# Performance work log

Measured on AMD Instinct MI355X. Metric: run time of the kernel, lower is better.

The kernel has to match this reference:

```python
import jax, jax.numpy as jnp
import numpy as np

NUM_NODES = 50000
NUM_GRAPHS = 64
HIDDEN = 256
F_IN = 256
NUM_EDGES = 800000


def setup_inputs() -> dict:
    key = jax.random.key(0)
    ks = jax.random.split(key, 8)
    x = jax.random.normal(ks[0], (NUM_NODES, F_IN), dtype=jnp.float32)
    edge_index = jax.random.randint(ks[1], (2, NUM_EDGES), 0, NUM_NODES, dtype=jnp.int64)
    batch = jnp.sort(jax.random.randint(ks[2], (NUM_NODES,), 0, NUM_GRAPHS, dtype=jnp.int64))
    # Glorot-ish init for weights, zeros for biases (as PyG GCNConv / Linear defaults)
    s1 = 1.0 / np.sqrt(F_IN)
    s2 = 1.0 / np.sqrt(HIDDEN)
    W1 = jax.random.uniform(ks[3], (F_IN, HIDDEN), jnp.float32, -s1, s1)
    b1 = jnp.zeros((HIDDEN,), jnp.float32)
    W2 = jax.random.uniform(ks[4], (HIDDEN, HIDDEN), jnp.float32, -s2, s2)
    b2 = jnp.zeros((HIDDEN,), jnp.float32)
    W_out = jax.random.uniform(ks[5], (HIDDEN, 1), jnp.float32, -s2, s2)
    b_out = jnp.zeros((1,), jnp.float32)
    return {"x": x, "edge_index": edge_index, "batch": batch,
            "W1": W1, "b1": b1, "W2": W2, "b2": b2,
            "W_out": W_out, "b_out": b_out}


def gcn_conv(x, W, b, src, dst, num_nodes):
    """GCNConv with added self-loops and symmetric D^{-1/2} A D^{-1/2} norm."""
    # degrees over edges incl. self-loops (src/dst already include them)
    deg = jax.ops.segment_sum(jnp.ones_like(src, dtype=x.dtype), dst,
                              num_segments=num_nodes)
    dinv = jax.lax.rsqrt(jnp.maximum(deg, 1e-12))
    norm = dinv[src] * dinv[dst]                       # [E+N]
    h = x @ W                                           # [N, H] dense GEMM
    msg = h[src] * norm[:, None]                        # gather + scale
    out = jax.ops.segment_sum(msg, dst, num_segments=num_nodes)  # scatter-add
    return out + b


def reference(x, edge_index, batch, W1, b1, W2, b2, W_out, b_out):
    n = x.shape[0]
    loops = jnp.arange(n, dtype=edge_index.dtype)
    src = jnp.concatenate([edge_index[0], loops])
    dst = jnp.concatenate([edge_index[1], loops])
    h = jax.nn.relu(gcn_conv(x, W1, b1, src, dst, n))
    h = jax.nn.relu(gcn_conv(h, W2, b2, src, dst, n))
    pooled = jax.ops.segment_sum(h, batch, num_segments=NUM_GRAPHS)  # [G, H]
    return pooled @ W_out + b_out
```

## Files before the change

### kernel.cpp

```cpp
#include <hip/hip_runtime.h>
#include <hip/hip_fp16.h>

#define N_NODES 50000
#define NFEAT   256
#define NGRAPH  64
#define NEDGE   800000
#define NBLK_SCAN 196
#define NBLK_M  196

typedef __attribute__((ext_vector_type(8))) _Float16 half8;
typedef __attribute__((ext_vector_type(2))) _Float16 h2v;
typedef __attribute__((ext_vector_type(4))) float f32x4;

static __device__ __forceinline__ float h2f(unsigned short u) {
    return __half2float(__ushort_as_half(u));
}
static __device__ __forceinline__ unsigned short f2h(float f) {
    return __half_as_ushort(__float2half(f));
}

__global__ void k_count(const int* __restrict__ dst, int* __restrict__ cnt) {
    int e = blockIdx.x * 256 + threadIdx.x;
    if (e < NEDGE) atomicAdd(&cnt[dst[e]], 1);
}

__global__ __launch_bounds__(256) void k_scan1(const int* __restrict__ cnt,
                                               int* __restrict__ row_start,
                                               int* __restrict__ bsum) {
    const int t = threadIdx.x, i = blockIdx.x * 256 + t;
    const int lane = t & 63, w = t >> 6;
    const int c = (i < N_NODES) ? cnt[i] : 0;
    int incl = c;
#pragma unroll
    for (int off = 1; off < 64; off <<= 1) {
        int u = __shfl_up(incl, off, 64);
        if (lane >= off) incl += u;
    }
    __shared__ int wtot[4];
    if (lane == 63) wtot[w] = incl;
    __syncthreads();
    int wbase = 0;
#pragma unroll
    for (int k = 0; k < 4; ++k) wbase += (k < w) ? wtot[k] : 0;
    if (i < N_NODES) row_start[i] = wbase + incl - c;
    if (t == 255) bsum[blockIdx.x] = wbase + incl;
}

__global__ __launch_bounds__(256) void k_scan2(int* __restrict__ bsum) {
    const int t = threadIdx.x, lane = t & 63, w = t >> 6;
    const int c = (t < NBLK_SCAN) ? bsum[t] : 0;
    int incl = c;
#pragma unroll
    for (int off = 1; off < 64; off <<= 1) {
        int u = __shfl_up(incl, off, 64);
        if (lane >= off) incl += u;
    }
    __shared__ int wtot[4];
    if (lane == 63) wtot[w] = incl;
    __syncthreads();
    int wbase = 0;
#pragma unroll
    for (int k = 0; k < 4; ++k) wbase += (k < w) ? wtot[k] : 0;
    if (t < NBLK_SCAN) bsum[t] = wbase + incl - c;
}

__global__ void k_scan3(int* __restrict__ row_start, const int* __restrict__ bsum,
                        int* __restrict__ cnt_cursor, float* __restrict__ dinv) {
    const int i = blockIdx.x * 256 + threadIdx.x;
    if (i >= N_NODES) return;
    const int c = cnt_cursor[i];
    const int start = row_start[i] + bsum[blockIdx.x];
    row_start[i] = start;
    cnt_cursor[i] = start;
    dinv[i] = rsqrtf((float)c + 1.0f);
    if (i == 0) row_start[N_NODES] = NEDGE;
}

__global__ void k_place(const int* __restrict__ src, const int* __restrict__ dst,
                        int* __restrict__ cursor, const float* __restrict__ dinv,
                        unsigned int* __restrict__ csr) {
    int e = blockIdx.x * 256 + threadIdx.x;
    if (e < NEDGE) {
        int s = src[e], d = dst[e];
        float norm = dinv[s] * dinv[d];
        int pos = atomicAdd(&cursor[d], 1);
        csr[pos] = ((unsigned int)f2h(norm) << 16) | (unsigned int)s;
    }
}

__global__ void k_prep_w(const float* __restrict__ W1, const float* __restrict__ W2,
                         unsigned short* __restrict__ w1t, unsigned short* __restrict__ w2t) {
    const int l = blockIdx.x >> 8;
    const int idx = (blockIdx.x & 255) * 256 + threadIdx.x;
    const int n = idx >> 8, k = idx & 255;
    const float* W = l ? W2 : W1;
    unsigned short* wt = l ? w2t : w1t;
    wt[n * 256 + k] = f2h(W[k * 256 + n]);
}

template <bool AF32>
__global__ __launch_bounds__(256) void k_gemm_mfma(const float* __restrict__ Af,
                                                   const unsigned short* __restrict__ Ah,
                                                   const unsigned short* __restrict__ Wt,
                                                   unsigned short* __restrict__ Ch, int M) {
    __shared__ unsigned short lds[32768];
    const int t = threadIdx.x;
    const int half = blockIdx.y;
    const int m0 = blockIdx.x * 256;
    const int w = t >> 6, lane = t & 63;
    const int lr = lane & 15, g = lane >> 4;

    {
        const unsigned short* wbase = Wt + (size_t)half * 128 * 256;
#pragma unroll
        for (int it = 0; it < 16; ++it) {
            const int unit = it * 256 + t;
            const int n = unit >> 5;
            const int rem = unit & 31;
            const int ks = rem >> 2, kg = rem & 3;
            const half8 v = *(const half8*)&wbase[n * 256 + rem * 8];
            const int kgx = kg ^ ((n >> 1) & 3);
            *(half8*)&lds[ks * 4096 + n * 32 + kgx * 8] = v;
        }
    }
    __syncthreads();

    const int rbase = m0 + w * 64;
    unsigned short* Chh = Ch + (size_t)half * (size_t)N_NODES * 128;

    half8 aA[8], aB[8];

#define LOADCHUNK(C, DST)                                                                \
    {                                                                                    \
        const int row = min(rbase + (C) * 16 + lr, M - 1);                               \
        _Pragma("unroll") for (int ks = 0; ks < 8; ++ks) {                               \
            if (AF32) {                                                                  \
                const float* ap = Af + (size_t)row * 256 + ks * 32 + g * 8;              \
                const float4 p0 = *(const float4*)ap;                                    \
                const float4 p1 = *(const float4*)(ap + 4);                              \
                half8 h;                                                                 \
                h[0] = (_Float16)p0.x; h[1] = (_Float16)p0.y;                            \
                h[2] = (_Float16)p0.z; h[3] = (_Float16)p0.w;                            \
                h[4] = (_Float16)p1.x; h[5] = (_Float16)p1.y;                            \
                h[6] = (_Float16)p1.z; h[7] = (_Float16)p1.w;                            \
                DST[ks] = h;                                                             \
            } else {                                                                     \
                DST[ks] = *(const half8*)(Ah + (size_t)(ks >> 2) * (size_t)N_NODES * 128 \
                                          + (size_t)row * 128 + (ks & 3) * 32 + g * 8);  \
            }                                                                            \
        }                                                                                \
    }

#define COMPUTE(C, SRC)                                                                  \
    {                                                                                    \
        f32x4 acc[8] = {};                                                               \
        _Pragma("unroll") for (int ks = 0; ks < 8; ++ks) {                               \
            _Pragma("unroll") for (int ni = 0; ni < 8; ++ni) {                           \
                const int n = ni * 16 + lr;                                              \
                const half8 bf = *(const half8*)&lds[ks * 4096 + n * 32 +                \
                                                     ((g ^ ((n >> 1) & 3)) << 3)];       \
                acc[ni] = __builtin_amdgcn_mfma_f32_16x16x32_f16(SRC[ks], bf,            \
                                                                 acc[ni], 0, 0, 0);      \
            }                                                                            \
        }                                                                                \
        const int r0 = rbase + (C) * 16 + g * 4;                                         \
        _Pragma("unroll") for (int ni = 0; ni < 8; ++ni) {                               \
            const int col = ni * 16 + lr;                                                \
            _Pragma("unroll") for (int r = 0; r < 4; ++r) {                              \
                if (r0 + r < M) Chh[(size_t)(r0 + r) * 128 + col] = f2h(acc[ni][r]);     \
            }                                                                            \
        }                                                                                \
    }

    LOADCHUNK(0, aA)
    LOADCHUNK(1, aB)
    COMPUTE(0, aA)
    LOADCHUNK(2, aA)
    COMPUTE(1, aB)
    LOADCHUNK(3, aB)
    COMPUTE(2, aA)
    COMPUTE(3, aB)

#undef LOADCHUNK
#undef COMPUTE
}

__global__ __launch_bounds__(256) void k_aggregate(const unsigned short* __restrict__ h16,
                                                   const int* __restrict__ row_start,
                                                   const unsigned int* __restrict__ csr,
                                                   const float* __restrict__ dinv,
                                                   const float* __restrict__ bias,
                                                   unsigned short* __restrict__ out) {
    const int wid = blockIdx.x * 4 + (threadIdx.x >> 6);
    if (wid >= 2 * N_NODES) return;
    const int half = (wid >= N_NODES) ? 1 : 0;
    const int node = wid - half * N_NODES;
    const int lane = threadIdx.x & 63;
    const int sub = lane >> 4;
    const int fl = lane & 15;
    const unsigned int* hu = (const unsigned int*)(h16 + (size_t)half * N_NODES * 128);

    float acc[8] = {};
    const int s0 = row_start[node], s1 = row_start[node + 1];
    const unsigned int* row = csr + s0;
    const int n = s1 - s0;

#define EDGEPAIR(EA, EB)                                                              \
    {                                                                                 \
        const unsigned int wnp = __builtin_amdgcn_perm(EB, EA, 0x07060302u);          \
        const h2v wn2 = __builtin_bit_cast(h2v, wnp);                                 \
        const uint4 va = *(const uint4*)(hu + (size_t)((EA)&0xffffu) * 64 + fl * 4);  \
        const uint4 vb = *(const uint4*)(hu + (size_t)((EB)&0xffffu) * 64 + fl * 4);  \
        unsigned int plo, phi;                                                        \
        plo = __builtin_amdgcn_perm(vb.x, va.x, 0x05040100u);                         \
        phi = __builtin_amdgcn_perm(vb.x, va.x, 0x07060302u);                         \
        acc[0] = __builtin_amdgcn_fdot2(__builtin_bit_cast(h2v, plo), wn2, acc[0], false); \
        acc[1] = __builtin_amdgcn_fdot2(__builtin_bit_cast(h2v, phi), wn2, acc[1], false); \
        plo = __builtin_amdgcn_perm(vb.y, va.y, 0x05040100u);                         \
        phi = __builtin_amdgcn_perm(vb.y, va.y, 0x07060302u);                         \
        acc[2] = __builtin_amdgcn_fdot2(__builtin_bit_cast(h2v, plo), wn2, acc[2], false); \
        acc[3] = __builtin_amdgcn_fdot2(__builtin_bit_cast(h2v, phi), wn2, acc[3], false); \
        plo = __builtin_amdgcn_perm(vb.z, va.z, 0x05040100u);                         \
        phi = __builtin_amdgcn_perm(vb.z, va.z, 0x07060302u);                         \
        acc[4] = __builtin_amdgcn_fdot2(__builtin_bit_cast(h2v, plo), wn2, acc[4], false); \
        acc[5] = __builtin_amdgcn_fdot2(__builtin_bit_cast(h2v, phi), wn2, acc[5], false); \
        plo = __builtin_amdgcn_perm(vb.w, va.w, 0x05040100u);                         \
        phi = __builtin_amdgcn_perm(vb.w, va.w, 0x07060302u);                         \
        acc[6] = __builtin_amdgcn_fdot2(__builtin_bit_cast(h2v, plo), wn2, acc[6], false); \
        acc[7] = __builtin_amdgcn_fdot2(__builtin_bit_cast(h2v, phi), wn2, acc[7], false); \
    }

    const int nfull = n & ~7;
    int j = 0;
    for (; j < nfull; j += 8) {
        const unsigned int ea = row[j + sub * 2];
        const unsigned int eb = row[j + sub * 2 + 1];
        EDGEPAIR(ea, eb)
    }
    if (j < n) {
        const int ia = j + sub * 2, ib = ia + 1;
        const unsigned int ea = (ia < n) ? row[ia] : 0u;
        const unsigned int eb = (ib < n) ? row[ib] : 0u;
        EDGEPAIR(ea, eb)
    }
#undef EDGEPAIR

#pragma unroll
    for (int i = 0; i < 8; ++i) {
        acc[i] += __shfl_xor(acc[i], 16, 64);
        acc[i] += __shfl_xor(acc[i], 32, 64);
    }

    if (sub == 0) {
        const float dd = dinv[node];
        const float ws = dd * dd;
        const uint4 sh = *(const uint4*)(hu + (size_t)node * 64 + fl * 4);
        const float4 b0 = *(const float4*)(bias + half * 128 + fl * 8);
        const float4 b1 = *(const float4*)(bias + half * 128 + fl * 8 + 4);
        float r[8];
        r[0] = fmaf(h2f((unsigned short)(sh.x & 0xffff)), ws, acc[0]) + b0.x;
        r[1] = fmaf(h2f((unsigned short)(sh.x >> 16)),    ws, acc[1]) + b0.y;
        r[2] = fmaf(h2f((unsigned short)(sh.y & 0xffff)), ws, acc[2]) + b0.z;
        r[3] = fmaf(h2f((unsigned short)(sh.y >> 16)),    ws, acc[3]) + b0.w;
        r[4] = fmaf(h2f((unsigned short)(sh.z & 0xffff)), ws, acc[4]) + b1.x;
        r[5] = fmaf(h2f((unsigned short)(sh.z >> 16)),    ws, acc[5]) + b1.y;
        r[6] = fmaf(h2f((unsigned short)(sh.w & 0xffff)), ws, acc[6]) + b1.z;
        r[7] = fmaf(h2f((unsigned short)(sh.w >> 16)),    ws, acc[7]) + b1.w;
#pragma unroll
        for (int i = 0; i < 8; ++i) r[i] = fmaxf(r[i], 0.f);
        uint4 o;
        o.x = (unsigned int)f2h(r[0]) | ((unsigned int)f2h(r[1]) << 16);
        o.y = (unsigned int)f2h(r[2]) | ((unsigned int)f2h(r[3]) << 16);
        o.z = (unsigned int)f2h(r[4]) | ((unsigned int)f2h(r[5]) << 16);
        o.w = (unsigned int)f2h(r[6]) | ((unsigned int)f2h(r[7]) << 16);
        *(uint4*)((unsigned int*)(out + (size_t)half * N_NODES * 128) +
                  (size_t)node * 64 + fl * 4) = o;
    }
}

__global__ void k_pool(const unsigned short* __restrict__ h2, const int* __restrict__ batch,
                       float* __restrict__ pooled) {
    const int strip = blockIdx.x * 2 + (threadIdx.x >> 7);
    const int tf = threadIdx.x & 127;
    const int f = tf * 2;
    const unsigned short* base = h2 + (size_t)(f >> 7) * N_NODES * 128 + (f & 127);
    const int n0 = strip * 40, n1 = n0 + 40;
    int g = batch[n0];
    float ax = 0.f, ay = 0.f;
    for (int n = n0; n < n1; ++n) {
        const int bg = batch[n];
        if (bg != g) {
            unsafeAtomicAdd(&pooled[g * NFEAT + f], ax);
            unsafeAtomicAdd(&pooled[g * NFEAT + f + 1], ay);
            ax = ay = 0.f;
            g = bg;
        }
        const unsigned int u = *(const unsigned int*)(base + (size_t)n * 128);
        ax += h2f((unsigned short)(u & 0xffff));
        ay += h2f((unsigned short)(u >> 16));
    }
    unsafeAtomicAdd(&pooled[g * NFEAT + f], ax);
    unsafeAtomicAdd(&pooled[g * NFEAT + f + 1], ay);
}

__global__ void k_final(const float* __restrict__ pooled, const float* __restrict__ Wout,
                        const float* __restrict__ bout, float* __restrict__ out) {
    const int g = blockIdx.x, t = threadIdx.x;
    float v = pooled[g * NFEAT + t] * Wout[t];
#pragma unroll
    for (int off = 32; off > 0; off >>= 1) v += __shfl_down(v, off, 64);
    __shared__ float sred[4];
    if ((t & 63) == 0) sred[t >> 6] = v;
    __syncthreads();
    if (t == 0) out[g] = sred[0] + sred[1] + sred[2] + sred[3] + bout[0];
}

extern "C" void kernel_launch(void* const* d_in, const int* in_sizes, int n_in,
                              void* d_out, int out_size, void* d_ws, size_t ws_size,
                              hipStream_t stream) {
    const float* x     = (const float*)d_in[0];
    const int*   ei    = (const int*)d_in[1];
    const int*   batch = (const int*)d_in[2];
    const float* W1    = (const float*)d_in[3];
    const float* b1    = (const float*)d_in[4];
    const float* W2    = (const float*)d_in[5];
    const float* b2    = (const float*)d_in[6];
    const float* Wout  = (const float*)d_in[7];
    const float* bout  = (const float*)d_in[8];
    float* out = (float*)d_out;

    const int* srcp = ei;
    const int* dstp = ei + NEDGE;

    const size_t NE128 = (size_t)N_NODES * 128;
    unsigned short* hA = (unsigned short*)d_ws;
    unsigned short* hB = hA + 2 * NE128;
    float* dinv      = (float*)(hB + 2 * NE128);
    float* pooled    = dinv + N_NODES;
    int*   cnt       = (int*)(pooled + NGRAPH * NFEAT);
    int*   row_start = cnt + N_NODES;
    int*   bsum      = row_start + N_NODES + 3;
    unsigned int* csr = (unsigned int*)(bsum + 256);
    unsigned short* w1t = (unsigned short*)(csr + NEDGE);
    unsigned short* w2t = w1t + 65536;

    const int nblk_edges = (NEDGE + 255) / 256;

    hipMemsetAsync(cnt, 0, N_NODES * sizeof(int), stream);
    k_count<<<nblk_edges, 256, 0, stream>>>(dstp, cnt);
    k_scan1<<<NBLK_SCAN, 256, 0, stream>>>(cnt, row_start, bsum);
    k_scan2<<<1, 256, 0, stream>>>(bsum);
    k_scan3<<<NBLK_SCAN, 256, 0, stream>>>(row_start, bsum, cnt, dinv);
    k_place<<<nblk_edges, 256, 0, stream>>>(srcp, dstp, cnt, dinv, csr);

    k_prep_w<<<512, 256, 0, stream>>>(W1, W2, w1t, w2t);

    const dim3 ggrid(NBLK_M, 2);
    const int agg_grid = (2 * N_NODES + 3) / 4;

    k_gemm_mfma<true><<<ggrid, 256, 0, stream>>>(x, nullptr, w1t, hA, N_NODES);
    k_aggregate<<<agg_grid, 256, 0, stream>>>(hA, row_start, csr, dinv, b1, hB);

    k_gemm_mfma<false><<<ggrid, 256, 0, stream>>>(nullptr, hB, w2t, hA, N_NODES);
    k_aggregate<<<agg_grid, 256, 0, stream>>>(hA, row_start, csr, dinv, b2, hB);

    hipMemsetAsync(pooled, 0, NGRAPH * NFEAT * sizeof(float), stream);
    k_pool<<<625, 256, 0, stream>>>(hB, batch, pooled);
    k_final<<<NGRAPH, 256, 0, stream>>>(pooled, Wout, bout, out);
}
```

Measured before the change: 280.7 us.

## Pre-convert x to fp16 and restructure MFMA GEMM to 512 threads with transposed output

Adds a separate kernel that converts x to fp16 in the split-half layout, so the first GEMM reads fp16 like the second. The GEMM goes from 256 to 512 threads per block, each wave handling 32 rows instead of 64, with both A chunks loaded up front. Swapping the MFMA operands puts each lane's four results along columns, so one 8-byte store replaces four scattered 2-byte stores. The extra conversion pass adds a full read of x and a write of an fp16 copy, and the larger workspace needs more memory.

After: 299.5 us. 6.7% more time.

```diff
diff --git a/kernel.cpp b/kernel.cpp
--- a/kernel.cpp
+++ b/kernel.cpp
@@ -11,6 +11,7 @@
 typedef __attribute__((ext_vector_type(8))) _Float16 half8;
 typedef __attribute__((ext_vector_type(2))) _Float16 h2v;
 typedef __attribute__((ext_vector_type(4))) float f32x4;
+struct alignas(8) US4 { unsigned short x, y, z, w; };
 
 static __device__ __forceinline__ float h2f(unsigned short u) {
     return __half2float(__ushort_as_half(u));
@@ -98,11 +99,25 @@
     wt[n * 256 + k] = f2h(W[k * 256 + n]);
 }
 
-template <bool AF32>
-__global__ __launch_bounds__(256) void k_gemm_mfma(const float* __restrict__ Af,
-                                                   const unsigned short* __restrict__ Ah,
-                                                   const unsigned short* __restrict__ Wt,
-                                                   unsigned short* __restrict__ Ch, int M) {
+__global__ void k_half_x(const float* __restrict__ x, unsigned short* __restrict__ hx) {
+    const int idx = blockIdx.x * 256 + threadIdx.x;
+    if (idx >= N_NODES * 32) return;
+    const int node = idx >> 5, sub = idx & 31;
+    const int half = sub >> 4, fl = sub & 15;
+    const float* ap = x + (size_t)node * 256 + half * 128 + fl * 8;
+    const float4 p0 = *(const float4*)ap;
+    const float4 p1 = *(const float4*)(ap + 4);
+    half8 h;
+    h[0] = (_Float16)p0.x; h[1] = (_Float16)p0.y;
+    h[2] = (_Float16)p0.z; h[3] = (_Float16)p0.w;
+    h[4] = (_Float16)p1.x; h[5] = (_Float16)p1.y;
+    h[6] = (_Float16)p1.z; h[7] = (_Float16)p1.w;
+    *(half8*)(hx + (size_t)half * N_NODES * 128 + (size_t)node * 128 + fl * 8) = h;
+}
+
+__global__ __launch_bounds__(512, 4) void k_gemm_mfma(const unsigned short* __restrict__ Ah,
+                                                      const unsigned short* __restrict__ Wt,
+                                                      unsigned short* __restrict__ Ch, int M) {
     __shared__ unsigned short lds[32768];
     const int t = threadIdx.x;
     const int half = blockIdx.y;
@@ -113,8 +128,8 @@
     {
         const unsigned short* wbase = Wt + (size_t)half * 128 * 256;
 #pragma unroll
-        for (int it = 0; it < 16; ++it) {
-            const int unit = it * 256 + t;
+        for (int it = 0; it < 8; ++it) {
+            const int unit = it * 512 + t;
             const int n = unit >> 5;
             const int rem = unit & 31;
             const int ks = rem >> 2, kg = rem & 3;
@@ -125,33 +140,24 @@
     }
     __syncthreads();
 
-    const int rbase = m0 + w * 64;
+    const int rbase = m0 + w * 32;
+    const unsigned short* Ahh = Ah + (size_t)0;
     unsigned short* Chh = Ch + (size_t)half * (size_t)N_NODES * 128;
 
+    const int row0 = min(rbase + lr, M - 1);
+    const int row1 = min(rbase + 16 + lr, M - 1);
+
     half8 aA[8], aB[8];
-
-#define LOADCHUNK(C, DST)                                                                \
-    {                                                                                    \
-        const int row = min(rbase + (C) * 16 + lr, M - 1);                               \
-        _Pragma("unroll") for (int ks = 0; ks < 8; ++ks) {                               \
-            if (AF32) {                                                                  \
-                const float* ap = Af + (size_t)row * 256 + ks * 32 + g * 8;              \
-                const float4 p0 = *(const float4*)ap;                                    \
-                const float4 p1 = *(const float4*)(ap + 4);                              \
-                half8 h;                                                                 \
-                h[0] = (_Float16)p0.x; h[1] = (_Float16)p0.y;                            \
-                h[2] = (_Float16)p0.z; h[3] = (_Float16)p0.w;                            \
-                h[4] = (_Float16)p1.x; h[5] = (_Float16)p1.y;                            \
-                h[6] = (_Float16)p1.z; h[7] = (_Float16)p1.w;                            \
-                DST[ks] = h;                                                             \
-            } else {                                                                     \
-                DST[ks] = *(const half8*)(Ah + (size_t)(ks >> 2) * (size_t)N_NODES * 128 \
-                                          + (size_t)row * 128 + (ks & 3) * 32 + g * 8);  \
-            }                                                                            \
-        }                                                                                \
-    }
-
-#define COMPUTE(C, SRC)                                                                  \
+#pragma unroll
+    for (int ks = 0; ks < 8; ++ks)
+        aA[ks] = *(const half8*)(Ahh + (size_t)(ks >> 2) * (size_t)N_NODES * 128 +
+                                 (size_t)row0 * 128 + (ks & 3) * 32 + g * 8);
+#pragma unroll
+    for (int ks = 0; ks < 8; ++ks)
+        aB[ks] = *(const half8*)(Ahh + (size_t)(ks >> 2) * (size_t)N_NODES * 128 +
+                                 (size_t)row1 * 128 + (ks & 3) * 32 + g * 8);
+
+#define COMPUTE(ROW, SRC)                                                                \
     {                                                                                    \
         f32x4 acc[8] = {};                                                               \
         _Pragma("unroll") for (int ks = 0; ks < 8; ++ks) {                               \
@@ -159,29 +165,24 @@
                 const int n = ni * 16 + lr;                                              \
                 const half8 bf = *(const half8*)&lds[ks * 4096 + n * 32 +                \
                                                      ((g ^ ((n >> 1) & 3)) << 3)];       \
-                acc[ni] = __builtin_amdgcn_mfma_f32_16x16x32_f16(SRC[ks], bf,            \
+                acc[ni] = __builtin_amdgcn_mfma_f32_16x16x32_f16(bf, SRC[ks],            \
                                                                  acc[ni], 0, 0, 0);      \
             }                                                                            \
         }                                                                                \
-        const int r0 = rbase + (C) * 16 + g * 4;                                         \
-        _Pragma("unroll") for (int ni = 0; ni < 8; ++ni) {                               \
-            const int col = ni * 16 + lr;                                                \
-            _Pragma("unroll") for (int r = 0; r < 4; ++r) {                              \
-                if (r0 + r < M) Chh[(size_t)(r0 + r) * 128 + col] = f2h(acc[ni][r]);     \
+        if ((ROW) < M) {                                                                 \
+            _Pragma("unroll") for (int ni = 0; ni < 8; ++ni) {                           \
+                US4 o;                                                                   \
+                o.x = f2h(acc[ni][0]); o.y = f2h(acc[ni][1]);                            \
+                o.z = f2h(acc[ni][2]); o.w = f2h(acc[ni][3]);                            \
+                *(US4*)(Chh + (size_t)(ROW)*128 + ni * 16 + g * 4) = o;                  \
             }                                                                            \
         }                                                                                \
     }
 
-    LOADCHUNK(0, aA)
-    LOADCHUNK(1, aB)
-    COMPUTE(0, aA)
-    LOADCHUNK(2, aA)
-    COMPUTE(1, aB)
-    LOADCHUNK(3, aB)
-    COMPUTE(2, aA)
-    COMPUTE(3, aB)
-
-#undef LOADCHUNK
+    const int srow0 = rbase + lr;
+    const int srow1 = rbase + 16 + lr;
+    COMPUTE(srow0, aA)
+    COMPUTE(srow1, aB)
 #undef COMPUTE
 }
 
@@ -335,7 +336,8 @@
     const size_t NE128 = (size_t)N_NODES * 128;
     unsigned short* hA = (unsigned short*)d_ws;
     unsigned short* hB = hA + 2 * NE128;
-    float* dinv      = (float*)(hB + 2 * NE128);
+    unsigned short* hX = hB + 2 * NE128;
+    float* dinv      = (float*)(hX + 2 * NE128);
     float* pooled    = dinv + N_NODES;
     int*   cnt       = (int*)(pooled + NGRAPH * NFEAT);
     int*   row_start = cnt + N_NODES;
@@ -354,14 +356,15 @@
     k_place<<<nblk_edges, 256, 0, stream>>>(srcp, dstp, cnt, dinv, csr);
 
     k_prep_w<<<512, 256, 0, stream>>>(W1, W2, w1t, w2t);
+    k_half_x<<<(N_NODES * 32 + 255) / 256, 256, 0, stream>>>(x, hX);
 
     const dim3 ggrid(NBLK_M, 2);
     const int agg_grid = (2 * N_NODES + 3) / 4;
 
-    k_gemm_mfma<true><<<ggrid, 256, 0, stream>>>(x, nullptr, w1t, hA, N_NODES);
+    k_gemm_mfma<<<ggrid, 512, 0, stream>>>(hX, w1t, hA, N_NODES);
     k_aggregate<<<agg_grid, 256, 0, stream>>>(hA, row_start, csr, dinv, b1, hB);
 
-    k_gemm_mfma<false><<<ggrid, 256, 0, stream>>>(nullptr, hB, w2t, hA, N_NODES);
+    k_gemm_mfma<<<ggrid, 512, 0, stream>>>(hB, w2t, hA, N_NODES);
     k_aggregate<<<agg_grid, 256, 0, stream>>>(hA, row_start, csr, dinv, b2, hB);
 
     hipMemsetAsync(pooled, 0, NGRAPH * NFEAT * sizeof(float), stream);
```
